# Kernel optimization log

Hardware: AMD Instinct MI355X
Metric: run time of the kernel (lower is better)

The kernel has to match this reference:

```python
import jax, jax.numpy as jnp
import numpy as np

N_EMBD = 1024
N_HEAD = 16
D_K = N_EMBD // N_HEAD
B, T = 2, 2048
NEG = -10000000000.0


def setup_inputs() -> dict:
    key = jax.random.key(0)
    ks = jax.random.split(key, 9)
    s = 1.0 / np.sqrt(N_EMBD)
    mk = lambda k: jax.random.uniform(k, (N_EMBD, N_EMBD), jnp.float32, -s, s)
    mb = lambda k: jax.random.uniform(k, (N_EMBD,), jnp.float32, -s, s)
    return {
        "x": jax.random.normal(ks[0], (B, T, N_EMBD), jnp.float32),
        "Wq": mk(ks[1]), "bq": mb(ks[2]),
        "Wk": mk(ks[3]), "bk": mb(ks[4]),
        "Wv": mk(ks[5]), "bv": mb(ks[6]),
        "Wo": mk(ks[7]), "bo": mb(ks[8]),
    }


def reference(x, Wq, bq, Wk, bk, Wv, bv, Wo, bo):
    Bx, Tx, _ = x.shape
    split = lambda h: h.reshape(Bx, Tx, N_HEAD, D_K).transpose(0, 2, 1, 3)  # [B,H,T,d_k]
    q = split(x @ Wq.T + bq)
    k = split(x @ Wk.T + bk)
    v = split(x @ Wv.T + bv)
    scores = jnp.einsum("bhqd,bhkd->bhqk", q, k) / np.sqrt(D_K)
    causal = jnp.tril(jnp.ones((Tx, Tx), dtype=bool))
    scores = jnp.where(causal[None, None], scores, NEG)
    prob = jax.nn.softmax(scores, axis=-1)
    y = jnp.einsum("bhqk,bhkd->bhqd", prob, v)
    y = y.transpose(0, 2, 1, 3).reshape(Bx, Tx, N_EMBD)
    return y @ Wo.T + bo
```

## Files before the change

### kernel.cpp

```cpp
#include <hip/hip_runtime.h>
#include <hip/hip_bf16.h>

#define N_EMBD 1024
#define T_SEQ  2048
#define BATCH  2
#define NHEAD  16
#define DKH    64
#define MTOK   (BATCH * T_SEQ)

typedef __attribute__((ext_vector_type(8))) short short8;
typedef __attribute__((ext_vector_type(4))) short short4v;
typedef __attribute__((ext_vector_type(4))) float floatx4;

#define QSCALE 0.18033688011112042f

static __device__ __forceinline__ short bf16_of(float f) {
    union { float f; unsigned u; } x; x.f = f;
    unsigned r = (x.u + 0x7fff + ((x.u >> 16) & 1)) >> 16;
    return (short)r;
}


__global__ __launch_bounds__(256) void cvt_frag(
    const float* __restrict__ x,  const float* __restrict__ Wq,
    const float* __restrict__ Wk, const float* __restrict__ Wv,
    const float* __restrict__ Wo,
    short* __restrict__ xf, short* __restrict__ wqkf,
    short* __restrict__ wvf, short* __restrict__ wof)
{
    int b = blockIdx.x;
    const float* src; short* dst; int srb, drb;
    if (b < 256)      { src = x;  dst = xf;   srb = b;       drb = srb; }
    else if (b < 320) { src = Wq; dst = wqkf; srb = b - 256; drb = srb; }
    else if (b < 384) { src = Wk; dst = wqkf; srb = b - 320; drb = srb + 64; }
    else if (b < 448) { src = Wv; dst = wvf;  srb = b - 384; drb = srb; }
    else              { src = Wo; dst = wof;  srb = b - 448; drb = srb; }

    const int row16 = threadIdx.x >> 4;
    const int kseg  = (threadIdx.x & 15) * 64;
    const float* sp = src + ((long)srb * 16 + row16) * 1024 + kseg;
    short* dp       = dst + ((long)drb * 32 + (kseg >> 5)) * 512 + row16 * 8;

#pragma unroll
    for (int c = 0; c < 8; ++c) {
        float4 v0 = *(const float4*)(sp + c * 8);
        float4 v1 = *(const float4*)(sp + c * 8 + 4);
        short8 o;
        o[0] = bf16_of(v0.x); o[1] = bf16_of(v0.y); o[2] = bf16_of(v0.z); o[3] = bf16_of(v0.w);
        o[4] = bf16_of(v1.x); o[5] = bf16_of(v1.y); o[6] = bf16_of(v1.z); o[7] = bf16_of(v1.w);
        *(short8*)(dp + (c >> 2) * 512 + (c & 3) * 128) = o;
    }
}

#define GEMM_KLOOP(Ab, Bb)                                                     \
    floatx4 acc[4][8] = {};                                                    \
    short8 a0[4], a1[4], b0[8], b1[8];                                         \
    _Pragma("unroll") for (int i = 0; i < 4; ++i)                              \
        a0[i] = *(const short8*)(Ab + (long)i * 32 * 512);                     \
    _Pragma("unroll") for (int j = 0; j < 8; ++j)                              \
        b0[j] = *(const short8*)(Bb + (long)j * 32 * 512);                     \
    for (int kc = 0; kc < 32; kc += 2) {                                       \
        __builtin_amdgcn_s_barrier();                                          \
        _Pragma("unroll") for (int i = 0; i < 4; ++i)                          \
            a1[i] = *(const short8*)(Ab + ((long)i * 32 + kc + 1) * 512);      \
        _Pragma("unroll") for (int j = 0; j < 8; ++j)                          \
            b1[j] = *(const short8*)(Bb + ((long)j * 32 + kc + 1) * 512);      \
        _Pragma("unroll") for (int i = 0; i < 4; ++i)                          \
            _Pragma("unroll") for (int j = 0; j < 8; ++j)                      \
                acc[i][j] = __builtin_amdgcn_mfma_f32_16x16x32_bf16(           \
                    a0[i], b0[j], acc[i][j], 0, 0, 0);                         \
        if (kc + 2 < 32) {                                                     \
            _Pragma("unroll") for (int i = 0; i < 4; ++i)                      \
                a0[i] = *(const short8*)(Ab + ((long)i * 32 + kc + 2) * 512);  \
            _Pragma("unroll") for (int j = 0; j < 8; ++j)                      \
                b0[j] = *(const short8*)(Bb + ((long)j * 32 + kc + 2) * 512);  \
        }                                                                      \
        _Pragma("unroll") for (int i = 0; i < 4; ++i)                          \
            _Pragma("unroll") for (int j = 0; j < 8; ++j)                      \
                acc[i][j] = __builtin_amdgcn_mfma_f32_16x16x32_bf16(           \
                    a1[i], b1[j], acc[i][j], 0, 0, 0);                         \
    }

__global__ __launch_bounds__(128, 2) void gemm_qkv(
    const short* __restrict__ xf, const short* __restrict__ wqkf,
    const short* __restrict__ wvf,
    const float* __restrict__ bq, const float* __restrict__ bk, const float* __restrict__ bv,
    short* __restrict__ outQ, short* __restrict__ outK, short* __restrict__ outV)
{
    const int lane = threadIdx.x & 63;
    const int w    = threadIdx.x >> 6;
    const int quad = lane >> 4, lr = lane & 15;
    const int bid  = blockIdx.x;
    const bool isQK = bid < 512;
    int mw, nw;
    const short *Af, *Bf;
    if (isQK) { mw = ((bid >> 5) * 2 + w) * 64;  nw = (bid & 31) * 128; Af = wqkf; Bf = xf; }
    else      { int v = bid - 512;
                mw = ((v >> 3) * 2 + w) * 64;    nw = (v & 7) * 128;    Af = xf;   Bf = wvf; }

    const short* Ab = Af + (long)(mw >> 4) * 32 * 512 + lane * 8;
    const short* Bb = Bf + (long)(nw >> 4) * 32 * 512 + lane * 8;

    GEMM_KLOOP(Ab, Bb)

    if (isQK) {
#pragma unroll
        for (int i = 0; i < 4; ++i) {
#pragma unroll
            for (int j = 0; j < 8; ++j) {
                int f0  = mw + i * 16 + quad * 4;
                int t   = nw + j * 16 + lr;
                int tb  = t & 2047;
                int sel = f0 >> 10;
                int fb  = f0 & 1023;
                int h   = fb >> 6, d0 = fb & 63;
                long bh = (long)(t >> 11) * NHEAD + h;
                float4 bias = *(const float4*)((sel ? bk : bq) + fb);
                short4v y;
#pragma unroll
                for (int r = 0; r < 4; ++r) {
                    float v = acc[i][j][r] + (&bias.x)[r];
                    if (sel == 0) v *= QSCALE;
                    y[r] = bf16_of(v);
                }
                long idx = ((bh * 128 + (tb >> 4)) * 2 + (d0 >> 5)) * 512
                         + (((d0 >> 3) & 3) * 16 + (tb & 15)) * 8 + (d0 & 7);
                *(short4v*)((sel ? outK : outQ) + idx) = y;
            }
        }
    } else {
#pragma unroll
        for (int i = 0; i < 4; ++i) {
#pragma unroll
            for (int j = 0; j < 8; ++j) {
                int t0 = mw + i * 16 + quad * 4;
                int tb = t0 & 2047;
                int d  = nw + j * 16 + lr;
                int h  = d >> 6, dblk = (d >> 4) & 3;
                long bh = (long)(t0 >> 11) * NHEAD + h;
                float bias = bv[d];
                short4v y;
#pragma unroll
                for (int r = 0; r < 4; ++r) y[r] = bf16_of(acc[i][j][r] + bias);
                long idx = ((bh * 64 + (tb >> 5)) * 4 + dblk) * 512
                         + lane * 8 + (i & 1) * 4;
                *(short4v*)(outV + idx) = y;
            }
        }
    }
}

__global__ __launch_bounds__(128, 2) void gemm_proj(
    const short* __restrict__ Yf, const short* __restrict__ wof,
    const float* __restrict__ bo, float* __restrict__ out)
{
    const int lane = threadIdx.x & 63;
    const int w    = threadIdx.x >> 6;
    const int quad = lane >> 4, lr = lane & 15;
    const int bid  = blockIdx.x;
    const int mw   = ((bid >> 5) * 2 + w) * 64;
    const int nw   = (bid & 31) * 128;

    const short* Ab = wof + (long)(mw >> 4) * 32 * 512 + lane * 8;
    const short* Bb = Yf  + (long)(nw >> 4) * 32 * 512 + lane * 8;

    GEMM_KLOOP(Ab, Bb)

#pragma unroll
    for (int i = 0; i < 4; ++i) {
#pragma unroll
        for (int j = 0; j < 8; ++j) {
            int  f0 = mw + i * 16 + quad * 4;
            long t  = nw + j * 16 + lr;
            float4 b4 = *(const float4*)(bo + f0);
            float4 o4;
            o4.x = acc[i][j][0] + b4.x;
            o4.y = acc[i][j][1] + b4.y;
            o4.z = acc[i][j][2] + b4.z;
            o4.w = acc[i][j][3] + b4.w;
            *(float4*)(out + t * N_EMBD + f0) = o4;
        }
    }
}

__global__ __launch_bounds__(256) void attn_kernel(
    const short* __restrict__ Qf, const short* __restrict__ Kf,
    const short* __restrict__ Vf, short* __restrict__ Y)
{
    __shared__ float Ob[2][32][68];
    __shared__ float Lb[2][32];

    const int tid  = threadIdx.x;
    const int w    = tid >> 6, lane = tid & 63;
    const int quad = lane >> 4, lr = lane & 15;
    const int qs   = w & 1, half = w >> 1;

    const int id = blockIdx.x;
    const int qt = 31 - (id >> 5);
    const int bh = id & 31;

    const short* Qp = Qf + (long)bh * 131072;
    const short* Kp = Kf + (long)bh * 131072;
    const short* Vp = Vf + (long)bh * 131072;

    const int qrb = qt * 64 + qs * 32;
    const int qb  = qrb >> 4;

    short8 qfv[2][2];
#pragma unroll
    for (int m = 0; m < 2; ++m)
#pragma unroll
        for (int c = 0; c < 2; ++c)
            qfv[m][c] = *(const short8*)(Qp + (long)(((qb + m) * 2 + c) * 512) + lane * 8);

    floatx4 o[2][4] = {};
    float rs[2] = {0.f, 0.f};

    const int S_tot = 2 * qt + qs + 1;
    const int h0 = (S_tot + 1) >> 1;
    const int sb = half ? h0 : 0;
    const int se = half ? S_tot : h0;

    short8 kbn[2][2];
    short8 vbn[4];
    if (sb < se) {
#pragma unroll
        for (int blk = 0; blk < 2; ++blk)
#pragma unroll
            for (int c = 0; c < 2; ++c)
                kbn[blk][c] = *(const short8*)(Kp + (long)(((sb * 2 + blk) * 2 + c) * 512) + lane * 8);
#pragma unroll
        for (int d = 0; d < 4; ++d)
            vbn[d] = *(const short8*)(Vp + (long)((sb * 4 + d) * 512) + lane * 8);
    }

    for (int s = sb; s < se; ++s) {
        short8 ka[2][2];
        short8 va[4];
#pragma unroll
        for (int blk = 0; blk < 2; ++blk)
#pragma unroll
            for (int c = 0; c < 2; ++c) ka[blk][c] = kbn[blk][c];
#pragma unroll
        for (int d = 0; d < 4; ++d) va[d] = vbn[d];

        if (s + 1 < se) {
#pragma unroll
            for (int blk = 0; blk < 2; ++blk)
#pragma unroll
                for (int c = 0; c < 2; ++c)
                    kbn[blk][c] = *(const short8*)(Kp + (long)((((s + 1) * 2 + blk) * 2 + c) * 512) + lane * 8);
#pragma unroll
            for (int d = 0; d < 4; ++d)
                vbn[d] = *(const short8*)(Vp + (long)(((s + 1) * 4 + d) * 512) + lane * 8);
        }

        floatx4 sc[2][2];
        __builtin_amdgcn_s_setprio(1);
#pragma unroll
        for (int m = 0; m < 2; ++m)
#pragma unroll
            for (int blk = 0; blk < 2; ++blk) {
                floatx4 z = {};
                z = __builtin_amdgcn_mfma_f32_16x16x32_bf16(ka[blk][0], qfv[m][0], z, 0, 0, 0);
                z = __builtin_amdgcn_mfma_f32_16x16x32_bf16(ka[blk][1], qfv[m][1], z, 0, 0, 0);
                sc[m][blk] = z;
            }
        __builtin_amdgcn_s_setprio(0);

        if (s == S_tot - 1) {
            const int k0 = s * 32;
#pragma unroll
            for (int m = 0; m < 2; ++m)
#pragma unroll
                for (int blk = 0; blk < 2; ++blk)
#pragma unroll
                    for (int r = 0; r < 4; ++r) {
                        int key = k0 + blk * 16 + quad * 4 + r;
                        if (key > qrb + m * 16 + lr) sc[m][blk][r] = -INFINITY;
                    }
        }

        short8 pa[2];
#pragma unroll
        for (int m = 0; m < 2; ++m) {
            union { short8 v; short e[8]; } pu;
#pragma unroll
            for (int blk = 0; blk < 2; ++blk)
#pragma unroll
                for (int r = 0; r < 4; ++r) {
                    float p = __builtin_amdgcn_exp2f(sc[m][blk][r]);
                    rs[m] += p;
                    union { float f; unsigned u; } cc; cc.f = p;
                    pu.e[blk * 4 + r] = (short)((cc.u + 0x8000u) >> 16);
                }
            pa[m] = pu.v;
        }

        __builtin_amdgcn_s_setprio(1);
#pragma unroll
        for (int m = 0; m < 2; ++m)
#pragma unroll
            for (int d = 0; d < 4; ++d)
                o[m][d] = __builtin_amdgcn_mfma_f32_16x16x32_bf16(va[d], pa[m], o[m][d], 0, 0, 0);
        __builtin_amdgcn_s_setprio(0);
    }

#pragma unroll
    for (int m = 0; m < 2; ++m) {
        rs[m] += __shfl_xor(rs[m], 16, 64);
        rs[m] += __shfl_xor(rs[m], 32, 64);
    }

    if (half == 1) {
#pragma unroll
        for (int m = 0; m < 2; ++m) {
#pragma unroll
            for (int d = 0; d < 4; ++d)
                *(floatx4*)&Ob[qs][m * 16 + lr][d * 16 + quad * 4] = o[m][d];
            Lb[qs][m * 16 + lr] = rs[m];
        }
    }
    __syncthreads();
    if (half == 0) {
        const long rb0 = (long)(bh >> 4) * 128 + qb;
        const int  hk  = (bh & 15) * DKH;
#pragma unroll
        for (int m = 0; m < 2; ++m) {
            float l   = rs[m] + Lb[qs][m * 16 + lr];
            float inv = 1.f / l;
            long  rb  = rb0 + m;
#pragma unroll
            for (int d = 0; d < 4; ++d) {
                floatx4 ob = *(const floatx4*)&Ob[qs][m * 16 + lr][d * 16 + quad * 4];
                short4v y4;
#pragma unroll
                for (int r = 0; r < 4; ++r) y4[r] = bf16_of((o[m][d][r] + ob[r]) * inv);
                int kb = hk + d * 16 + quad * 4;
                long idx = (rb * 32 + (kb >> 5)) * 512
                         + (((kb >> 3) & 3) * 16 + lr) * 8 + (quad & 1) * 4;
                *(short4v*)(Y + idx) = y4;
            }
        }
    }
}

extern "C" void kernel_launch(void* const* d_in, const int* in_sizes, int n_in,
                              void* d_out, int out_size, void* d_ws, size_t ws_size,
                              hipStream_t stream) {
    const float* x  = (const float*)d_in[0];
    const float* Wq = (const float*)d_in[1];
    const float* bq = (const float*)d_in[2];
    const float* Wk = (const float*)d_in[3];
    const float* bk = (const float*)d_in[4];
    const float* Wv = (const float*)d_in[5];
    const float* bv = (const float*)d_in[6];
    const float* Wo = (const float*)d_in[7];
    const float* bo = (const float*)d_in[8];
    float* out = (float*)d_out;

    char* ws = (char*)d_ws;
    short* xf   = (short*)(ws);
    short* wqkf = (short*)(ws + (8L  << 20));
    short* wvf  = (short*)(ws + (12L << 20));
    short* wof  = (short*)(ws + (14L << 20));
    short* Qb   = (short*)(ws + (16L << 20));
    short* Kbuf = (short*)(ws + (24L << 20));
    short* Vtb  = (short*)(ws + (32L << 20));
    short* Yf   = xf;

    cvt_frag<<<512, 256, 0, stream>>>(x, Wq, Wk, Wv, Wo, xf, wqkf, wvf, wof);

    gemm_qkv<<<768, 128, 0, stream>>>(xf, wqkf, wvf, bq, bk, bv, Qb, Kbuf, Vtb);
    attn_kernel<<<1024, 256, 0, stream>>>(Qb, Kbuf, Vtb, Yf);
    gemm_proj<<<256, 128, 0, stream>>>(Yf, wof, bo, out);
}
```

Baseline: 174.5 us.

## Stage GEMM tiles through LDS with direct global-to-LDS loads and 2x2 wave tiling

Measured after the change: 191.5 us. 1.1x slower.

```diff
diff --git a/kernel.cpp b/kernel.cpp
--- a/kernel.cpp
+++ b/kernel.cpp
@@ -18,6 +18,13 @@
     union { float f; unsigned u; } x; x.f = f;
     unsigned r = (x.u + 0x7fff + ((x.u >> 16) & 1)) >> 16;
     return (short)r;
+}
+
+static __device__ __forceinline__ void gload16(const short* g, short* l) {
+    __builtin_amdgcn_global_load_lds(
+        (const __attribute__((address_space(1))) unsigned int*)(g),
+        (__attribute__((address_space(3))) unsigned int*)(l),
+        16, 0, 0);
 }
 
 
@@ -52,36 +59,36 @@
     }
 }
 
-#define GEMM_KLOOP(Ab, Bb)                                                     \
-    floatx4 acc[4][8] = {};                                                    \
-    short8 a0[4], a1[4], b0[8], b1[8];                                         \
-    _Pragma("unroll") for (int i = 0; i < 4; ++i)                              \
-        a0[i] = *(const short8*)(Ab + (long)i * 32 * 512);                     \
-    _Pragma("unroll") for (int j = 0; j < 8; ++j)                              \
-        b0[j] = *(const short8*)(Bb + (long)j * 32 * 512);                     \
-    for (int kc = 0; kc < 32; kc += 2) {                                       \
-        __builtin_amdgcn_s_barrier();                                          \
-        _Pragma("unroll") for (int i = 0; i < 4; ++i)                          \
-            a1[i] = *(const short8*)(Ab + ((long)i * 32 + kc + 1) * 512);      \
-        _Pragma("unroll") for (int j = 0; j < 8; ++j)                          \
-            b1[j] = *(const short8*)(Bb + ((long)j * 32 + kc + 1) * 512);      \
-        _Pragma("unroll") for (int i = 0; i < 4; ++i)                          \
-            _Pragma("unroll") for (int j = 0; j < 8; ++j)                      \
-                acc[i][j] = __builtin_amdgcn_mfma_f32_16x16x32_bf16(           \
-                    a0[i], b0[j], acc[i][j], 0, 0, 0);                         \
-        if (kc + 2 < 32) {                                                     \
-            _Pragma("unroll") for (int i = 0; i < 4; ++i)                      \
-                a0[i] = *(const short8*)(Ab + ((long)i * 32 + kc + 2) * 512);  \
-            _Pragma("unroll") for (int j = 0; j < 8; ++j)                      \
-                b0[j] = *(const short8*)(Bb + ((long)j * 32 + kc + 2) * 512);  \
-        }                                                                      \
-        _Pragma("unroll") for (int i = 0; i < 4; ++i)                          \
-            _Pragma("unroll") for (int j = 0; j < 8; ++j)                      \
-                acc[i][j] = __builtin_amdgcn_mfma_f32_16x16x32_bf16(           \
-                    a1[i], b1[j], acc[i][j], 0, 0, 0);                         \
-    }
-
-__global__ __launch_bounds__(128, 2) void gemm_qkv(
+#define LDS_KLOOP(AfP, BfP, rb0, cb0)                                           \
+    __shared__ short lds[16 * 512];                                             \
+    floatx4 acc[4][4] = {};                                                     \
+    {                                                                           \
+        const int w_    = threadIdx.x >> 6;                                     \
+        const int lane_ = threadIdx.x & 63;                                     \
+        const int wr_   = w_ >> 1, wc_ = w_ & 1;                                \
+        const short* gb = (w_ < 2                                               \
+            ? (AfP) + (long)((rb0) + w_ * 4) * 32 * 512                         \
+            : (BfP) + (long)((cb0) + (w_ - 2) * 4) * 32 * 512) + lane_ * 8;     \
+        short* lb = &lds[w_ * 4 * 512];                                         \
+        for (int kb = 0; kb < 32; ++kb) {                                       \
+            _Pragma("unroll") for (int f = 0; f < 4; ++f)                       \
+                gload16(gb + ((long)f * 32 + kb) * 512, lb + f * 512);          \
+            asm volatile("s_waitcnt vmcnt(0)" ::: "memory");                    \
+            __syncthreads();                                                    \
+            short8 a_[4], b_[4];                                                \
+            _Pragma("unroll") for (int i = 0; i < 4; ++i)                       \
+                a_[i] = *(const short8*)&lds[(wr_ * 4 + i) * 512 + lane_ * 8];  \
+            _Pragma("unroll") for (int j = 0; j < 4; ++j)                       \
+                b_[j] = *(const short8*)&lds[(8 + wc_ * 4 + j) * 512 + lane_ * 8];\
+            _Pragma("unroll") for (int i = 0; i < 4; ++i)                       \
+                _Pragma("unroll") for (int j = 0; j < 4; ++j)                   \
+                    acc[i][j] = __builtin_amdgcn_mfma_f32_16x16x32_bf16(        \
+                        a_[i], b_[j], acc[i][j], 0, 0, 0);                      \
+            __syncthreads();                                                    \
+        }                                                                       \
+    }
+
+__global__ __launch_bounds__(256) void gemm_qkv(
     const short* __restrict__ xf, const short* __restrict__ wqkf,
     const short* __restrict__ wvf,
     const float* __restrict__ bq, const float* __restrict__ bk, const float* __restrict__ bv,
@@ -90,26 +97,30 @@
     const int lane = threadIdx.x & 63;
     const int w    = threadIdx.x >> 6;
     const int quad = lane >> 4, lr = lane & 15;
+    const int wr   = w >> 1, wc = w & 1;
+
     const int bid  = blockIdx.x;
     const bool isQK = bid < 512;
-    int mw, nw;
+    int mt, nt;
     const short *Af, *Bf;
-    if (isQK) { mw = ((bid >> 5) * 2 + w) * 64;  nw = (bid & 31) * 128; Af = wqkf; Bf = xf; }
+    if (isQK) { mt = bid >> 5;        nt = bid & 31; Af = wqkf; Bf = xf; }
     else      { int v = bid - 512;
-                mw = ((v >> 3) * 2 + w) * 64;    nw = (v & 7) * 128;    Af = xf;   Bf = wvf; }
-
-    const short* Ab = Af + (long)(mw >> 4) * 32 * 512 + lane * 8;
-    const short* Bb = Bf + (long)(nw >> 4) * 32 * 512 + lane * 8;
-
-    GEMM_KLOOP(Ab, Bb)
+                mt = v >> 3;          nt = v & 7;    Af = xf;   Bf = wvf; }
+
+    const int rb0 = mt * 8;
+    const int cb0 = nt * 8;
+    const int mwv = mt * 128 + wr * 64;
+    const int nwv = nt * 128 + wc * 64;
+
+    LDS_KLOOP(Af, Bf, rb0, cb0)
 
     if (isQK) {
 #pragma unroll
         for (int i = 0; i < 4; ++i) {
 #pragma unroll
-            for (int j = 0; j < 8; ++j) {
-                int f0  = mw + i * 16 + quad * 4;
-                int t   = nw + j * 16 + lr;
+            for (int j = 0; j < 4; ++j) {
+                int f0  = mwv + i * 16 + quad * 4;
+                int t   = nwv + j * 16 + lr;
                 int tb  = t & 2047;
                 int sel = f0 >> 10;
                 int fb  = f0 & 1023;
@@ -132,10 +143,10 @@
 #pragma unroll
         for (int i = 0; i < 4; ++i) {
 #pragma unroll
-            for (int j = 0; j < 8; ++j) {
-                int t0 = mw + i * 16 + quad * 4;
+            for (int j = 0; j < 4; ++j) {
+                int t0 = mwv + i * 16 + quad * 4;
                 int tb = t0 & 2047;
-                int d  = nw + j * 16 + lr;
+                int d  = nwv + j * 16 + lr;
                 int h  = d >> 6, dblk = (d >> 4) & 3;
                 long bh = (long)(t0 >> 11) * NHEAD + h;
                 float bias = bv[d];
@@ -150,28 +161,32 @@
     }
 }
 
-__global__ __launch_bounds__(128, 2) void gemm_proj(
+__global__ __launch_bounds__(256) void gemm_proj(
     const short* __restrict__ Yf, const short* __restrict__ wof,
     const float* __restrict__ bo, float* __restrict__ out)
 {
     const int lane = threadIdx.x & 63;
     const int w    = threadIdx.x >> 6;
     const int quad = lane >> 4, lr = lane & 15;
-    const int bid  = blockIdx.x;
-    const int mw   = ((bid >> 5) * 2 + w) * 64;
-    const int nw   = (bid & 31) * 128;
-
-    const short* Ab = wof + (long)(mw >> 4) * 32 * 512 + lane * 8;
-    const short* Bb = Yf  + (long)(nw >> 4) * 32 * 512 + lane * 8;
-
-    GEMM_KLOOP(Ab, Bb)
+    const int wr   = w >> 1, wc = w & 1;
+
+    const int bid = blockIdx.x;
+    const int mt  = bid >> 5;
+    const int nt  = bid & 31;
+
+    const int rb0 = mt * 8;
+    const int cb0 = nt * 8;
+    const int mwv = mt * 128 + wr * 64;
+    const int nwv = nt * 128 + wc * 64;
+
+    LDS_KLOOP(wof, Yf, rb0, cb0)
 
 #pragma unroll
     for (int i = 0; i < 4; ++i) {
 #pragma unroll
-        for (int j = 0; j < 8; ++j) {
-            int  f0 = mw + i * 16 + quad * 4;
-            long t  = nw + j * 16 + lr;
+        for (int j = 0; j < 4; ++j) {
+            int  f0 = mwv + i * 16 + quad * 4;
+            long t  = nwv + j * 16 + lr;
             float4 b4 = *(const float4*)(bo + f0);
             float4 o4;
             o4.x = acc[i][j][0] + b4.x;
@@ -371,7 +386,7 @@
 
     cvt_frag<<<512, 256, 0, stream>>>(x, Wq, Wk, Wv, Wo, xf, wqkf, wvf, wof);
 
-    gemm_qkv<<<768, 128, 0, stream>>>(xf, wqkf, wvf, bq, bk, bv, Qb, Kbuf, Vtb);
+    gemm_qkv<<<768, 256, 0, stream>>>(xf, wqkf, wvf, bq, bk, bv, Qb, Kbuf, Vtb);
     attn_kernel<<<1024, 256, 0, stream>>>(Qb, Kbuf, Vtb, Yf);
-    gemm_proj<<<256, 128, 0, stream>>>(Yf, wof, bo, out);
-}
+    gemm_proj<<<256, 256, 0, stream>>>(Yf, wof, bo, out);
+}
```
